# Kernel tuning notes

Hardware: AMD Instinct MI355X
Metric: run time of the kernel (lower is better)

Reference implementation:

```python
import jax, jax.numpy as jnp
import numpy as np

NTOKENS = 8192   # max_ntokens
TOPK = 2
H = 1024         # hidden
FFN = 4096       # ffn_hidden = 4*hidden
E = 8            # nexperts
M = NTOKENS * TOPK          # total dispatched rows (flux_m_max)
CAP = M // E                # balanced rows per expert


def setup_inputs() -> dict:
    key = jax.random.key(0)
    k1, k2, k3, k4 = jax.random.split(key, 4)
    x = jax.random.normal(k1, (NTOKENS, H), jnp.float32)
    weight0 = jax.random.normal(k2, (E, H, FFN), jnp.float32) * 0.02
    weight1 = jax.random.normal(k3, (E, FFN, H), jnp.float32) * 0.02
    # Balanced routing: scatter_index[t, k] is the row in the expert-sorted
    # dispatched buffer; a permutation of arange(M) gives exactly CAP rows/expert.
    scatter_index = jax.random.permutation(k4, M).reshape(NTOKENS, TOPK).astype(jnp.int32)
    splits = jnp.full((E,), CAP, dtype=jnp.int32)  # rows per expert, sum == M
    return {"x": x, "weight0": weight0, "weight1": weight1,
            "scatter_index": scatter_index, "splits": splits}


def reference(x, weight0, weight1, scatter_index, splits):
    ntokens, topk = scatter_index.shape
    n_exp, h, ffn = weight0.shape
    m = ntokens * topk
    cap = m // n_exp  # splits are balanced by construction (== splits[e])
    # --- AG-scatter: place each (token, k) replica at its dispatched row ---
    vals = jnp.repeat(x, topk, axis=0)                              # [M, h]
    dispatched = jnp.zeros((m, h), x.dtype).at[scatter_index.reshape(-1)].set(vals)
    xe = dispatched.reshape(n_exp, cap, h)                          # [E, C, h]
    # --- grouped GEMM 0 + exact GELU (torch F.gelu default = erf form) ---
    mid = jax.nn.gelu(jnp.einsum('ech,ehf->ecf', xe, weight0), approximate=False)
    # --- grouped GEMM 1 ---
    ye = jnp.einsum('ecf,efh->ech', mid, weight1).reshape(m, h)     # [M, h]
    # --- gather-RS: combine topk expert outputs per token ---
    return ye[scatter_index].sum(axis=1)                            # [ntokens, h]
```

## Files before the change

### kernel.cpp

```cpp
#include <hip/hip_runtime.h>
#include <hip/hip_bf16.h>
#include <cstdint>

constexpr int NT   = 8192;
constexpr int H    = 1024;
constexpr int FFN  = 4096;
constexpr int E    = 8;
constexpr int M    = NT * 2;
constexpr int CAP  = M / E;

typedef unsigned short u16;
typedef short short8 __attribute__((ext_vector_type(8)));
typedef float f32x4 __attribute__((ext_vector_type(4)));

__device__ __forceinline__ u16 f2bf(float f) {
  union { float f; unsigned u; } c{f};
  unsigned r = (c.u + 0x7FFFu + ((c.u >> 16) & 1u)) >> 16;
  return (u16)r;
}
__device__ __forceinline__ float bf2f(u16 u) {
  union { unsigned u; float f; } c{((unsigned)u) << 16};
  return c.f;
}
__device__ __forceinline__ void async16(const void* g, void* l) {
  auto gp = reinterpret_cast<const __attribute__((address_space(1))) unsigned*>(
      reinterpret_cast<uintptr_t>(g));
  auto lp = reinterpret_cast<__attribute__((address_space(3))) unsigned*>(
      reinterpret_cast<uintptr_t>(l));
  __builtin_amdgcn_global_load_lds(gp, lp, 16, 0, 0);
}

__device__ __forceinline__ float gelu_fast(float x) {
  const float u = x * x;
  const float w = x * (-2.30220795f + -0.102943895f * u);
  return x * __frcp_rn(1.0f + exp2f(w));
}

__device__ __forceinline__ void transpose_body(const float* __restrict__ W,
                                               u16* __restrict__ WT,
                                               int K, int N, int tb,
                                               float (*tile)[65]) {
  const int ntx = N >> 6;
  const int per = ntx * (K >> 6);
  const int e   = tb / per;
  const int rem = tb - e * per;
  const int bx  = rem % ntx;
  const int by  = rem / ntx;
  const float* Wp = W + (size_t)e * K * N;
  u16* Tp = WT + (size_t)e * K * N;
  const int k0 = by * 64, n0 = bx * 64;
  const int tid = threadIdx.x;

  const int u = tid & 15, krb = tid >> 4;
#pragma unroll
  for (int p = 0; p < 4; ++p) {
    const int kr = p * 16 + krb;
    float4 v = *(const float4*)&Wp[(size_t)(k0 + kr) * N + n0 + u * 4];
    tile[kr][u * 4 + 0] = v.x;
    tile[kr][u * 4 + 1] = v.y;
    tile[kr][u * 4 + 2] = v.z;
    tile[kr][u * 4 + 3] = v.w;
  }
  __syncthreads();

  const int n = tid >> 3, cb = tid & 7;
#pragma unroll
  for (int p = 0; p < 2; ++p) {
    const int nn = p * 32 + n;
    u16 pack[8];
#pragma unroll
    for (int j = 0; j < 8; ++j) pack[j] = f2bf(tile[cb * 8 + j][nn]);
    *(short8*)&Tp[(size_t)(n0 + nn) * K + k0 + cb * 8] = *(short8*)pack;
  }
}

__device__ __forceinline__ void scatter_body(const float* __restrict__ x,
                                             const int* __restrict__ sidx,
                                             u16* __restrict__ disp, int b) {
  const int tid = threadIdx.x;
  const int half = tid >> 7;
  const int r = tid & 127;
#pragma unroll
  for (int it = 0; it < 2; ++it) {
    const int t = it * 4096 + b * 2 + half;
    const int r0 = sidx[2 * t + 0];
    const int r1 = sidx[2 * t + 1];
    const float4* xr = (const float4*)(x + (size_t)t * H);
    float4 v0 = xr[r * 2 + 0];
    float4 v1 = xr[r * 2 + 1];
    u16 pk[8] = {f2bf(v0.x), f2bf(v0.y), f2bf(v0.z), f2bf(v0.w),
                 f2bf(v1.x), f2bf(v1.y), f2bf(v1.z), f2bf(v1.w)};
    *(short8*)&disp[(size_t)r0 * H + r * 8] = *(short8*)pk;
    *(short8*)&disp[(size_t)r1 * H + r * 8] = *(short8*)pk;
  }
}

__global__ __launch_bounds__(256)
void pre_kernel(const float* __restrict__ x, const float* __restrict__ w0,
                const float* __restrict__ w1, const int* __restrict__ sidx,
                u16* __restrict__ wt0, u16* __restrict__ wt1,
                u16* __restrict__ disp) {
  __shared__ float tile[64][65];
  const int b = blockIdx.x;
  if (b < 2048) { scatter_body(x, sidx, disp, b); return; }
  if (b < 10240) { transpose_body(w0, wt0, H, FFN, b - 2048, tile); return; }
  transpose_body(w1, wt1, FFN, H, b - 10240, tile);
}

__global__ __launch_bounds__(256)
void transpose_cvt_kernel(const float* __restrict__ W, u16* __restrict__ WT,
                          int K, int N) {
  __shared__ float tile[64][65];
  transpose_body(W, WT, K, N, blockIdx.x, tile);
}

template <bool GELU>
__global__ __launch_bounds__(512, 2)
void gemm_bt_kernel(const u16* __restrict__ A,
                    const u16* __restrict__ Bt,
                    u16* __restrict__ C,
                    int Mn, int Nn, int Kn, int ny) {
  __shared__ __align__(16) u16 lA[2 * 16384];
  __shared__ __align__(16) u16 lB[2 * 16384];

  const int b = blockIdx.x;
  const int e = b & 7;
  const int t = b >> 3;
  const int q = t & 15, s = t >> 4;
  const int sy = ny >> 2;
  const int sm = s % sy, sn = s / sy;
  const int tm = sm * 4 + (q & 3), tn = sn * 4 + (q >> 2);
  const int m0 = tm * 256, n0 = tn * 256;

  const u16* __restrict__ Ae = A  + (size_t)e * Mn * Kn + (size_t)m0 * Kn;
  const u16* __restrict__ Be = Bt + (size_t)e * Nn * Kn + (size_t)n0 * Kn;
  u16* __restrict__ Ce = C + (size_t)e * Mn * Nn;

  const int tid  = threadIdx.x;
  const int lane = tid & 63;
  const int wave = tid >> 6;
  const int wr = wave >> 2, wc = wave & 3;
  const int llo = lane & 15, lhi = lane >> 4, lsw = llo & 7;

  const int gcol = ((tid & 7) ^ ((tid >> 3) & 7)) * 8;
  const int rowA = tid >> 3;
  const int rowB = (wave >> 2) * 64 + (wave & 3) * 8 + ((tid >> 3) & 7);
  const u16* pA = Ae + (size_t)rowA * Kn + gcol;
  const u16* pB = Be + (size_t)rowB * Kn + gcol;
  const int ldA = wave * 8 * 64;
  const int ldB = ((wave >> 2) * 64 + (wave & 3) * 8) * 64;

  const int arow0 = (wr * 128 + llo) * 64;
  const int brow0 = (wc * 64 + llo) * 64;
  const int ck0 = (lhi ^ lsw) * 8;
  const int ck1 = ((lhi + 4) ^ lsw) * 8;

  const int KT  = Kn >> 6;
  const int KT4 = Kn >> 4;

  auto stage = [&](int n) {
    if (n >= KT4) return;
    const int mt = n >> 2, idx = n & 3;
    const int h = idx >> 1;
    const int koff = mt << 6;
    const int bsel = (mt & 1) << 14;
    if ((idx & 1) == 0) {
      const u16* sp = pA + (size_t)(h * 64) * Kn + koff;
      u16* dp = lA + bsel + h * (64 * 64) + ldA;
      async16(sp, dp);
      async16(sp + (size_t)128 * Kn, dp + 128 * 64);
    } else {
      const u16* sp = pB + (size_t)(h * 32) * Kn + koff;
      u16* dp = lB + bsel + h * (32 * 64) + ldB;
      async16(sp, dp);
      async16(sp + (size_t)128 * Kn, dp + 128 * 64);
    }
  };

  f32x4 acc[8][4] = {};
  short8 aA[4][2], b0f[2][2], b1f[2][2];

#pragma unroll
  for (int n = 0; n < 7; ++n) stage(n);
  asm volatile("s_waitcnt vmcnt(6)" ::: "memory");
  __builtin_amdgcn_s_barrier();

#pragma unroll 1
  for (int k = 0; k < KT; ++k) {
    const u16* bA = &lA[(k & 1) << 14];
    const u16* bB = &lB[(k & 1) << 14];
    const int g = 4 * k;

#pragma unroll
    for (int mi = 0; mi < 4; ++mi) {
      aA[mi][0] = *(const short8*)&bA[arow0 + mi * 1024 + ck0];
      aA[mi][1] = *(const short8*)&bA[arow0 + mi * 1024 + ck1];
    }
#pragma unroll
    for (int nj = 0; nj < 2; ++nj) {
      b0f[nj][0] = *(const short8*)&bB[brow0 + nj * 1024 + ck0];
      b0f[nj][1] = *(const short8*)&bB[brow0 + nj * 1024 + ck1];
    }
    stage(g + 7);
    asm volatile("s_waitcnt lgkmcnt(8)" ::: "memory");
    __builtin_amdgcn_s_barrier();
    asm volatile("s_waitcnt lgkmcnt(0)" ::: "memory");
    __builtin_amdgcn_s_setprio(1);
#pragma unroll
    for (int mi = 0; mi < 4; ++mi)
#pragma unroll
      for (int nj = 0; nj < 2; ++nj)
#pragma unroll
        for (int ks = 0; ks < 2; ++ks)
          acc[mi][nj] = __builtin_amdgcn_mfma_f32_16x16x32_bf16(
              aA[mi][ks], b0f[nj][ks], acc[mi][nj], 0, 0, 0);
    __builtin_amdgcn_s_setprio(0);
    __builtin_amdgcn_s_barrier();

#pragma unroll
    for (int nj = 0; nj < 2; ++nj) {
      b1f[nj][0] = *(const short8*)&bB[brow0 + (nj + 2) * 1024 + ck0];
      b1f[nj][1] = *(const short8*)&bB[brow0 + (nj + 2) * 1024 + ck1];
    }
    stage(g + 8);
    __builtin_amdgcn_s_barrier();
    asm volatile("s_waitcnt lgkmcnt(0)" ::: "memory");
    __builtin_amdgcn_s_setprio(1);
#pragma unroll
    for (int mi = 0; mi < 4; ++mi)
#pragma unroll
      for (int nj = 0; nj < 2; ++nj)
#pragma unroll
        for (int ks = 0; ks < 2; ++ks)
          acc[mi][nj + 2] = __builtin_amdgcn_mfma_f32_16x16x32_bf16(
              aA[mi][ks], b1f[nj][ks], acc[mi][nj + 2], 0, 0, 0);
    __builtin_amdgcn_s_setprio(0);
    __builtin_amdgcn_s_barrier();

#pragma unroll
    for (int mi = 0; mi < 4; ++mi) {
      aA[mi][0] = *(const short8*)&bA[arow0 + (mi + 4) * 1024 + ck0];
      aA[mi][1] = *(const short8*)&bA[arow0 + (mi + 4) * 1024 + ck1];
    }
    stage(g + 9);
    __builtin_amdgcn_s_barrier();
    asm volatile("s_waitcnt lgkmcnt(0)" ::: "memory");
    __builtin_amdgcn_s_setprio(1);
#pragma unroll
    for (int mi = 0; mi < 4; ++mi)
#pragma unroll
      for (int nj = 0; nj < 2; ++nj)
#pragma unroll
        for (int ks = 0; ks < 2; ++ks)
          acc[mi + 4][nj + 2] = __builtin_amdgcn_mfma_f32_16x16x32_bf16(
              aA[mi][ks], b1f[nj][ks], acc[mi + 4][nj + 2], 0, 0, 0);
    __builtin_amdgcn_s_setprio(0);
    __builtin_amdgcn_s_barrier();

    stage(g + 10);
    __builtin_amdgcn_s_barrier();
    __builtin_amdgcn_s_setprio(1);
#pragma unroll
    for (int mi = 0; mi < 4; ++mi)
#pragma unroll
      for (int nj = 0; nj < 2; ++nj)
#pragma unroll
        for (int ks = 0; ks < 2; ++ks)
          acc[mi + 4][nj] = __builtin_amdgcn_mfma_f32_16x16x32_bf16(
              aA[mi][ks], b0f[nj][ks], acc[mi + 4][nj], 0, 0, 0);
    __builtin_amdgcn_s_setprio(0);

    if (k + 2 < KT) {
      asm volatile("s_waitcnt vmcnt(6)" ::: "memory");
      __builtin_amdgcn_s_barrier();
    } else if (k + 2 == KT) {
      asm volatile("s_waitcnt vmcnt(0)" ::: "memory");
      __builtin_amdgcn_s_barrier();
    }
  }

#pragma unroll
  for (int mi = 0; mi < 8; ++mi) {
    const int mrow = m0 + wr * 128 + mi * 16 + lhi * 4;
#pragma unroll
    for (int nj = 0; nj < 4; ++nj) {
      const int ncol = n0 + wc * 64 + nj * 16 + llo;
#pragma unroll
      for (int r = 0; r < 4; ++r) {
        float v = acc[mi][nj][r];
        if (GELU) v = gelu_fast(v);
        Ce[(size_t)(mrow + r) * Nn + ncol] = f2bf(v);
      }
    }
  }
}

__global__ __launch_bounds__(256)
void gather_sum_kernel(const u16* __restrict__ ye,
                       const int* __restrict__ sidx,
                       float* __restrict__ out) {
  const int tid = threadIdx.x;
  const int half = tid >> 7;
  const int r = tid & 127;
#pragma unroll
  for (int it = 0; it < 2; ++it) {
    const int t = it * 4096 + blockIdx.x * 2 + half;
    const int r0 = sidx[2 * t + 0];
    const int r1 = sidx[2 * t + 1];
    short8 a = *(const short8*)&ye[(size_t)r0 * H + r * 8];
    short8 b = *(const short8*)&ye[(size_t)r1 * H + r * 8];
    float4 s0, s1;
    s0.x = bf2f((u16)a[0]) + bf2f((u16)b[0]);
    s0.y = bf2f((u16)a[1]) + bf2f((u16)b[1]);
    s0.z = bf2f((u16)a[2]) + bf2f((u16)b[2]);
    s0.w = bf2f((u16)a[3]) + bf2f((u16)b[3]);
    s1.x = bf2f((u16)a[4]) + bf2f((u16)b[4]);
    s1.y = bf2f((u16)a[5]) + bf2f((u16)b[5]);
    s1.z = bf2f((u16)a[6]) + bf2f((u16)b[6]);
    s1.w = bf2f((u16)a[7]) + bf2f((u16)b[7]);
    float4* orow = (float4*)(out + (size_t)t * H);
    orow[r * 2 + 0] = s0;
    orow[r * 2 + 1] = s1;
  }
}

extern "C" void kernel_launch(void* const* d_in, const int* in_sizes, int n_in,
                              void* d_out, int out_size, void* d_ws, size_t ws_size,
                              hipStream_t stream) {
  (void)in_sizes; (void)n_in; (void)out_size;
  const float* x    = (const float*)d_in[0];
  const float* w0   = (const float*)d_in[1];
  const float* w1   = (const float*)d_in[2];
  const int*   sidx = (const int*)d_in[3];
  float* out = (float*)d_out;

  char* ws = (char*)d_ws;
  const size_t MB = 1024ull * 1024;
  u16* wt0  = (u16*)ws;
  u16* wt1  = (u16*)(ws + 64 * MB);
  u16* disp = (u16*)(ws + 128 * MB);
  u16* mid  = (u16*)(ws + 160 * MB);
  u16* ye   = disp;
  const bool roomy = ws_size >= 288 * MB;

  if (roomy) {
    pre_kernel<<<18432, 256, 0, stream>>>(x, w0, w1, sidx, wt0, wt1, disp);
    gemm_bt_kernel<true><<<1024, 512, 0, stream>>>(disp, wt0, mid, CAP, FFN, H, CAP / 256);
    gemm_bt_kernel<false><<<256, 512, 0, stream>>>(mid, wt1, ye, CAP, H, FFN, CAP / 256);
  } else {
    wt1 = wt0;
    pre_kernel<<<10240, 256, 0, stream>>>(x, w0, w1, sidx, wt0, wt1, disp);
    gemm_bt_kernel<true><<<1024, 512, 0, stream>>>(disp, wt0, mid, CAP, FFN, H, CAP / 256);
    transpose_cvt_kernel<<<8192, 256, 0, stream>>>(w1, wt1, FFN, H);
    gemm_bt_kernel<false><<<256, 512, 0, stream>>>(mid, wt1, ye, CAP, H, FFN, CAP / 256);
  }
  gather_sum_kernel<<<2048, 256, 0, stream>>>(ye, sidx, out);
}
```

Before: 614.0 us.

## Make GEMM0 persistent over four N tiles and split pre_kernel into separate launches

```diff
diff --git a/kernel.cpp b/kernel.cpp
--- a/kernel.cpp
+++ b/kernel.cpp
@@ -74,9 +74,11 @@
   }
 }
 
-__device__ __forceinline__ void scatter_body(const float* __restrict__ x,
-                                             const int* __restrict__ sidx,
-                                             u16* __restrict__ disp, int b) {
+__global__ __launch_bounds__(256)
+void scatter_kernel(const float* __restrict__ x,
+                    const int* __restrict__ sidx,
+                    u16* __restrict__ disp) {
+  const int b = blockIdx.x;
   const int tid = threadIdx.x;
   const int half = tid >> 7;
   const int r = tid & 127;
@@ -96,44 +98,33 @@
 }
 
 __global__ __launch_bounds__(256)
-void pre_kernel(const float* __restrict__ x, const float* __restrict__ w0,
-                const float* __restrict__ w1, const int* __restrict__ sidx,
-                u16* __restrict__ wt0, u16* __restrict__ wt1,
-                u16* __restrict__ disp) {
-  __shared__ float tile[64][65];
-  const int b = blockIdx.x;
-  if (b < 2048) { scatter_body(x, sidx, disp, b); return; }
-  if (b < 10240) { transpose_body(w0, wt0, H, FFN, b - 2048, tile); return; }
-  transpose_body(w1, wt1, FFN, H, b - 10240, tile);
-}
-
-__global__ __launch_bounds__(256)
 void transpose_cvt_kernel(const float* __restrict__ W, u16* __restrict__ WT,
                           int K, int N) {
   __shared__ float tile[64][65];
   transpose_body(W, WT, K, N, blockIdx.x, tile);
 }
 
-template <bool GELU>
+template <bool GELU, int KTLOG, int NSEG>
 __global__ __launch_bounds__(512, 2)
 void gemm_bt_kernel(const u16* __restrict__ A,
                     const u16* __restrict__ Bt,
                     u16* __restrict__ C,
-                    int Mn, int Nn, int Kn, int ny) {
+                    int Mn, int Nn, int Kn) {
   __shared__ __align__(16) u16 lA[2 * 16384];
   __shared__ __align__(16) u16 lB[2 * 16384];
 
+  constexpr int KT = 1 << KTLOG;
+  constexpr int TT = NSEG * KT;
+
   const int b = blockIdx.x;
   const int e = b & 7;
-  const int t = b >> 3;
-  const int q = t & 15, s = t >> 4;
-  const int sy = ny >> 2;
-  const int sm = s % sy, sn = s / sy;
-  const int tm = sm * 4 + (q & 3), tn = sn * 4 + (q >> 2);
-  const int m0 = tm * 256, n0 = tn * 256;
+  const int p = b >> 3;
+  const int tm  = p & 7;
+  const int tn0 = (p >> 3) * NSEG;
+  const int m0 = tm * 256;
 
   const u16* __restrict__ Ae = A  + (size_t)e * Mn * Kn + (size_t)m0 * Kn;
-  const u16* __restrict__ Be = Bt + (size_t)e * Nn * Kn + (size_t)n0 * Kn;
+  const u16* __restrict__ Be = Bt + (size_t)e * Nn * Kn + (size_t)tn0 * 256 * Kn;
   u16* __restrict__ Ce = C + (size_t)e * Mn * Nn;
 
   const int tid  = threadIdx.x;
@@ -155,22 +146,21 @@
   const int ck0 = (lhi ^ lsw) * 8;
   const int ck1 = ((lhi + 4) ^ lsw) * 8;
 
-  const int KT  = Kn >> 6;
-  const int KT4 = Kn >> 4;
-
   auto stage = [&](int n) {
-    if (n >= KT4) return;
-    const int mt = n >> 2, idx = n & 3;
+    if (n >= 4 * TT) return;
+    const int gt  = n >> 2, idx = n & 3;
+    const int seg = gt >> KTLOG;
+    const int kofs = (gt & (KT - 1)) << 6;
+    const int bsel = (gt & 1) << 14;
     const int h = idx >> 1;
-    const int koff = mt << 6;
-    const int bsel = (mt & 1) << 14;
     if ((idx & 1) == 0) {
-      const u16* sp = pA + (size_t)(h * 64) * Kn + koff;
+      const u16* sp = pA + (size_t)(h * 64) * Kn + kofs;
       u16* dp = lA + bsel + h * (64 * 64) + ldA;
       async16(sp, dp);
       async16(sp + (size_t)128 * Kn, dp + 128 * 64);
     } else {
-      const u16* sp = pB + (size_t)(h * 32) * Kn + koff;
+      const u16* sp = pB + (size_t)seg * 256 * (size_t)Kn +
+                      (size_t)(h * 32) * Kn + kofs;
       u16* dp = lB + bsel + h * (32 * 64) + ldB;
       async16(sp, dp);
       async16(sp + (size_t)128 * Kn, dp + 128 * 64);
@@ -180,16 +170,39 @@
   f32x4 acc[8][4] = {};
   short8 aA[4][2], b0f[2][2], b1f[2][2];
 
+  auto epilogue = [&](int seg) {
+    const int n0 = (tn0 + seg) * 256;
+#pragma unroll
+    for (int mi = 0; mi < 8; ++mi) {
+      const int mrow = m0 + wr * 128 + mi * 16 + lhi * 4;
+#pragma unroll
+      for (int nj = 0; nj < 4; ++nj) {
+        const int ncol = n0 + wc * 64 + nj * 16 + llo;
+#pragma unroll
+        for (int r = 0; r < 4; ++r) {
+          float v = acc[mi][nj][r];
+          if (GELU) v = gelu_fast(v);
+          Ce[(size_t)(mrow + r) * Nn + ncol] = f2bf(v);
+        }
+      }
+    }
+    const f32x4 z = {0.f, 0.f, 0.f, 0.f};
+#pragma unroll
+    for (int mi = 0; mi < 8; ++mi)
+#pragma unroll
+      for (int nj = 0; nj < 4; ++nj) acc[mi][nj] = z;
+  };
+
 #pragma unroll
   for (int n = 0; n < 7; ++n) stage(n);
   asm volatile("s_waitcnt vmcnt(6)" ::: "memory");
   __builtin_amdgcn_s_barrier();
 
 #pragma unroll 1
-  for (int k = 0; k < KT; ++k) {
-    const u16* bA = &lA[(k & 1) << 14];
-    const u16* bB = &lB[(k & 1) << 14];
-    const int g = 4 * k;
+  for (int gt = 0; gt < TT; ++gt) {
+    const u16* bA = &lA[(gt & 1) << 14];
+    const u16* bB = &lB[(gt & 1) << 14];
+    const int g = 4 * gt;
 
 #pragma unroll
     for (int mi = 0; mi < 4; ++mi) {
@@ -270,28 +283,15 @@
               aA[mi][ks], b0f[nj][ks], acc[mi + 4][nj], 0, 0, 0);
     __builtin_amdgcn_s_setprio(0);
 
-    if (k + 2 < KT) {
+    if (gt + 2 < TT) {
       asm volatile("s_waitcnt vmcnt(6)" ::: "memory");
       __builtin_amdgcn_s_barrier();
-    } else if (k + 2 == KT) {
+    } else if (gt + 2 == TT) {
       asm volatile("s_waitcnt vmcnt(0)" ::: "memory");
       __builtin_amdgcn_s_barrier();
     }
-  }
-
-#pragma unroll
-  for (int mi = 0; mi < 8; ++mi) {
-    const int mrow = m0 + wr * 128 + mi * 16 + lhi * 4;
-#pragma unroll
-    for (int nj = 0; nj < 4; ++nj) {
-      const int ncol = n0 + wc * 64 + nj * 16 + llo;
-#pragma unroll
-      for (int r = 0; r < 4; ++r) {
-        float v = acc[mi][nj][r];
-        if (GELU) v = gelu_fast(v);
-        Ce[(size_t)(mrow + r) * Nn + ncol] = f2bf(v);
-      }
-    }
+
+    if ((gt & (KT - 1)) == (KT - 1)) epilogue(gt >> KTLOG);
   }
 }
 
@@ -344,15 +344,18 @@
   const bool roomy = ws_size >= 288 * MB;
 
   if (roomy) {
-    pre_kernel<<<18432, 256, 0, stream>>>(x, w0, w1, sidx, wt0, wt1, disp);
-    gemm_bt_kernel<true><<<1024, 512, 0, stream>>>(disp, wt0, mid, CAP, FFN, H, CAP / 256);
-    gemm_bt_kernel<false><<<256, 512, 0, stream>>>(mid, wt1, ye, CAP, H, FFN, CAP / 256);
+    scatter_kernel<<<2048, 256, 0, stream>>>(x, sidx, disp);
+    transpose_cvt_kernel<<<8192, 256, 0, stream>>>(w0, wt0, H, FFN);
+    transpose_cvt_kernel<<<8192, 256, 0, stream>>>(w1, wt1, FFN, H);
+    gemm_bt_kernel<true, 4, 4><<<256, 512, 0, stream>>>(disp, wt0, mid, CAP, FFN, H);
+    gemm_bt_kernel<false, 6, 1><<<256, 512, 0, stream>>>(mid, wt1, ye, CAP, H, FFN);
   } else {
     wt1 = wt0;
-    pre_kernel<<<10240, 256, 0, stream>>>(x, w0, w1, sidx, wt0, wt1, disp);
-    gemm_bt_kernel<true><<<1024, 512, 0, stream>>>(disp, wt0, mid, CAP, FFN, H, CAP / 256);
+    scatter_kernel<<<2048, 256, 0, stream>>>(x, sidx, disp);
+    transpose_cvt_kernel<<<8192, 256, 0, stream>>>(w0, wt0, H, FFN);
+    gemm_bt_kernel<true, 4, 4><<<256, 512, 0, stream>>>(disp, wt0, mid, CAP, FFN, H);
     transpose_cvt_kernel<<<8192, 256, 0, stream>>>(w1, wt1, FFN, H);
-    gemm_bt_kernel<false><<<256, 512, 0, stream>>>(mid, wt1, ye, CAP, H, FFN, CAP / 256);
+    gemm_bt_kernel<false, 6, 1><<<256, 512, 0, stream>>>(mid, wt1, ye, CAP, H, FFN);
   }
   gather_sum_kernel<<<2048, 256, 0, stream>>>(ye, sidx, out);
 }
```

Measured after the change: 780.4 us. 27.1% more time.
